# Kernel optimization log

Measured on AMD Instinct MI355X. Metric: run time of the kernel, lower is better.

The kernel has to match this reference:

```python
import jax, jax.numpy as jnp
import numpy as np

MAX_FREQ = 10
CORR_RADIUS = 2
PATCH = 9


def _gelu(x):
    return jax.nn.gelu(x, approximate=False)


def _project(coords, R, C0, f, pp):
    # coords [N,3] -> uv [ncams,N,2], cam-space z [ncams,N]
    d = coords[None, :, :] - C0[:, None, :]
    Xc = jnp.einsum('cij,cnj->cni', R, d)
    z = jnp.maximum(Xc[..., 2:3], 1e-6)
    uv = Xc[..., :2] / z * f[:, None, :] + pp[:, None, :]
    return uv, Xc[..., 2]


def _fourier(x, max_freq):
    freqs = (2.0 ** jnp.arange(max_freq, dtype=x.dtype)) * jnp.pi
    xf = x[..., None] * freqs
    enc = jnp.concatenate([jnp.sin(xf), jnp.cos(xf)], axis=-1)  # [...,D,2F]
    return enc.reshape(enc.shape[:-2] + (x.shape[-1] * 2 * max_freq,))


def _bilinear_time(img, t, gx, gy):
    # img [B,T,C,H,W]; t [B,K] int; gx,gy [B,K,P] normalized grid in [-1,1]
    # grid_sample(align_corners=False, padding_mode='zeros') via direct 4-tap gather
    B, T, C, H, W = img.shape
    x = (gx + 1.0) * 0.5 * W - 0.5
    y = (gy + 1.0) * 0.5 * H - 0.5
    x0 = jnp.floor(x)
    y0 = jnp.floor(y)
    wx = (x - x0)[..., None]
    wy = (y - y0)[..., None]
    x0 = x0.astype(jnp.int32)
    y0 = y0.astype(jnp.int32)
    b = jnp.arange(B)[:, None, None]
    tt = t[:, :, None]

    def tap(yy, xx):
        ok = ((xx >= 0) & (xx < W) & (yy >= 0) & (yy < H))[..., None]
        v = img[b, tt, :, jnp.clip(yy, 0, H - 1), jnp.clip(xx, 0, W - 1)]  # [B,K,P,C]
        return v * ok.astype(v.dtype)

    return (tap(y0, x0) * (1 - wx) * (1 - wy) + tap(y0, x0 + 1) * wx * (1 - wy)
            + tap(y0 + 1, x0) * (1 - wx) * wy + tap(y0 + 1, x0 + 1) * wx * wy)


def _conv2d(x, w, b):
    y = jax.lax.conv_general_dilated(x, w, (1, 1), 'SAME', dimension_numbers=('NCHW', 'OIHW', 'NCHW'))
    return y + b[None, :, None, None]


def _conv3d(x, w, b):
    y = jax.lax.conv_general_dilated(x, w, (1, 1, 1), 'SAME', dimension_numbers=('NCDHW', 'OIDHW', 'NCDHW'))
    return y + b[None, :, None, None, None]


def reference(views, cam_R, cam_center, cam_focal, cam_pp, query_coords, query_time, target_time, cube_scale, v2v_w, v2v_b, lin_vol_w, lin_vol_b, lin_pos_w, lin_pos_b, lin_depth_w, lin_depth_b, conv1_w, conv1_b, conv2_w, conv2_b, conv3_w, conv3_b, mlp1_w, mlp1_b, mlp2_w, mlp2_b, tq_emb, tt_emb, vis_emb_tab, depth_norm_scale, gate_w, gate_b, fus1_w, fus1_b, fus2_w, fus2_b):
    ncams, B, T, C, H, W = views.shape
    K = query_coords.shape[1]
    sizes = jnp.asarray([W, H], dtype=query_coords.dtype)

    # project query points to all cameras
    qflat = query_coords.reshape(-1, 3)
    p2d_flat, zc = _project(qflat, cam_R, cam_center, cam_focal, cam_pp)  # [ncams,BK,2]
    p2d_full = p2d_flat.reshape(ncams, B, K, 2)

    # fourier position embedding
    pp_n = jnp.transpose(p2d_full, (1, 2, 0, 3)) / sizes  # [B,K,ncams,2]
    embed_pos = _fourier(pp_n, MAX_FREQ) @ lin_pos_w.T + lin_pos_b

    # volume embedding: masked multi-camera cube sampling + 3D conv
    cs = 2 * CORR_RADIUS + 1
    P3 = cs ** 3
    row = (jnp.arange(cs, dtype=query_coords.dtype) - CORR_RADIUS) * (cube_scale * 2.0)
    gx3, gy3, gz3 = jnp.meshgrid(row, row, row, indexing='ij')
    xyz = jnp.stack([gx3, gy3, gz3], axis=-1).reshape(-1, 3)  # [P3,3], x outermost
    cube = (query_coords[:, :, None, :] + xyz).reshape(-1, 3)
    pc, _ = _project(cube, cam_R, cam_center, cam_focal, cam_pp)
    pc = pc.reshape(ncams, B, K, P3, 2)
    smps, msks = [], []
    for c in range(ncams):
        g = 2.0 * pc[c] / sizes - 1.0
        m = (g[..., 0] >= -1) & (g[..., 0] <= 1) & (g[..., 1] >= -1) & (g[..., 1] <= 1)
        s = _bilinear_time(views[c], query_time, g[..., 0], g[..., 1])  # [B,K,P3,C]
        smps.append(s)
        msks.append(m)
    vol = jnp.stack(smps)  # [ncams,B,K,P3,C]
    mf = jnp.stack(msks).astype(vol.dtype)[..., None]
    cnt = jnp.maximum(mf.sum(0), 1.0)
    mv = (vol * mf).sum(0) / cnt  # [B,K,P3,C]
    mv = mv.reshape(B, K, cs, cs, cs, C)  # (x,y,z,C)
    mv = jnp.transpose(mv, (0, 1, 5, 4, 3, 2)).reshape(B * K, C, cs, cs, cs)  # [(BK),C,z,y,x]
    mv = _gelu(_conv3d(mv, v2v_w, v2v_b))  # EmbedV2V: Conv3d(3,vdim,3) + GELU
    vd = mv.shape[1]
    mv = mv.reshape(B, K, vd, cs, cs, cs)
    mv = jnp.transpose(mv, (0, 1, 2, 5, 4, 3)).reshape(B, K, vd * P3)  # 'b t 1 (d total)'
    embed_volume = mv @ lin_vol_w.T + lin_vol_b
    embed_volume = jnp.broadcast_to(embed_volume[:, :, None, :], (B, K, ncams, embed_volume.shape[-1]))

    # patch embedding per camera
    lin = jnp.arange(PATCH, dtype=query_coords.dtype)
    gyy, gxx = jnp.meshgrid(lin, lin, indexing='ij')
    offs = jnp.stack([gxx - (PATCH - 1) / 2.0, gyy - (PATCH - 1) / 2.0], axis=-1)  # [P,P,2]
    pats = []
    for c in range(ncams):
        px = p2d_full[c][:, :, None, None, :] + offs  # [B,K,P,P,2]
        g = ((2.0 * px + 1.0) / sizes - 1.0).reshape(B, K, PATCH * PATCH, 2)
        s = _bilinear_time(views[c], query_time, g[..., 0], g[..., 1])  # [B,K,PP,C]
        pats.append(jnp.transpose(s.reshape(B, K, PATCH, PATCH, C), (0, 1, 4, 2, 3)))
    patches = jnp.stack(pats).reshape(ncams * B * K, C, PATCH, PATCH)
    x = _gelu(_conv2d(patches, conv1_w, conv1_b))
    x = _gelu(_conv2d(x, conv2_w, conv2_b))
    x = _gelu(_conv2d(x, conv3_w, conv3_b))
    x = x.reshape(x.shape[0], -1)  # 'b c p q -> b (c p q)'
    x = _gelu(x @ mlp1_w.T + mlp1_b)  # dropout is eval-mode identity
    emb_p = x @ mlp2_w.T + mlp2_b
    embed_patch = jnp.transpose(emb_p.reshape(ncams, B, K, -1), (1, 2, 0, 3))

    E = tq_emb.shape[1]
    embed_qt = jnp.broadcast_to(tq_emb[query_time][:, :, None, :], (B, K, ncams, E))
    embed_tt = jnp.broadcast_to(tt_emb[target_time][:, :, None, :], (B, K, ncams, E))

    # visibility (pinhole in-bounds check with margin=2)
    u = p2d_flat[..., 0]
    v = p2d_flat[..., 1]
    margin = 2.0
    vis = (zc > 0) & (u >= margin) & (u <= W - margin) & (v >= margin) & (v <= H - margin)
    vis = jnp.transpose(vis.reshape(ncams, B, K), (1, 2, 0))  # [B,K,ncams]
    embed_vis = vis_emb_tab[vis.astype(jnp.int32)]

    depths = jnp.linalg.norm(query_coords[:, :, None, :] - cam_center, axis=-1) / (cube_scale * depth_norm_scale[0])
    embed_depth = _fourier(depths[..., None], MAX_FREQ) @ lin_depth_w.T + lin_depth_b

    # gated fusion of 7 terms + fusion MLP
    terms = [embed_pos, embed_volume, embed_patch, embed_qt, embed_tt, embed_vis, embed_depth]
    gates = jax.nn.sigmoid(jnp.concatenate(terms, axis=-1) @ gate_w.T + gate_b)  # [B,K,ncams,7]
    fused = sum(gates[..., i:i + 1] * terms[i] for i in range(len(terms)))
    h = _gelu(fused @ fus1_w.T + fus1_b)
    embed_total = h @ fus2_w.T + fus2_b  # [B,K,ncams,decoder_dim]
    return embed_total, vis


def setup_inputs():
    ks = jax.random.split(jax.random.key(0), 24)
    ncams, B, T, C, H, W = 4, 2, 16, 3, 256, 256
    K, E, MF, cs, P, vdim = 256, 256, 10, 5, 9, 8
    views = jax.random.normal(ks[0], (ncams, B, T, C, H, W), jnp.float32)
    cam_R = jnp.tile(jnp.eye(3, dtype=jnp.float32)[None], (ncams, 1, 1))
    cam_center = jnp.stack([jnp.linspace(-0.5, 0.5, ncams), jnp.linspace(0.5, -0.5, ncams), jnp.full((ncams,), -5.0)], axis=-1).astype(jnp.float32)
    cam_focal = jnp.full((ncams, 2), 200.0, jnp.float32)
    cam_pp = jnp.full((ncams, 2), 128.0, jnp.float32)
    query_coords = jax.random.uniform(ks[1], (B, K, 3), jnp.float32, -1.0, 1.0)
    query_time = jax.random.randint(ks[2], (B, K), 0, T).astype(jnp.int32)
    target_time = jax.random.randint(ks[3], (B, K), 0, T).astype(jnp.int32)
    cube_scale = jnp.float32(0.02)

    def w(k, shape, s=0.02):
        return jax.random.normal(k, shape, jnp.float32) * s

    z = lambda n: jnp.zeros((n,), jnp.float32)
    return dict(
        views=views, cam_R=cam_R, cam_center=cam_center, cam_focal=cam_focal, cam_pp=cam_pp,
        query_coords=query_coords, query_time=query_time, target_time=target_time, cube_scale=cube_scale,
        v2v_w=w(ks[4], (vdim, C, 3, 3, 3)), v2v_b=z(vdim),
        lin_vol_w=w(ks[5], (E, cs ** 3 * vdim)), lin_vol_b=z(E),
        lin_pos_w=w(ks[6], (E, 4 * MF)), lin_pos_b=z(E),
        lin_depth_w=w(ks[7], (E, 2 * MF)), lin_depth_b=z(E),
        conv1_w=w(ks[8], (32, 3, 3, 3)), conv1_b=z(32),
        conv2_w=w(ks[9], (64, 32, 3, 3)), conv2_b=z(64),
        conv3_w=w(ks[10], (128, 64, 3, 3)), conv3_b=z(128),
        mlp1_w=w(ks[11], (2 * E, 128 * P * P)), mlp1_b=z(2 * E),
        mlp2_w=w(ks[12], (E, 2 * E)), mlp2_b=z(E),
        tq_emb=w(ks[13], (T, E), 1.0), tt_emb=w(ks[14], (T, E), 1.0),
        vis_emb_tab=w(ks[15], (2, E), 1.0),
        depth_norm_scale=jnp.array([500.0], jnp.float32),
        gate_w=w(ks[16], (7, 7 * E), 0.01), gate_b=z(7),
        fus1_w=w(ks[17], (4 * E, E)), fus1_b=z(4 * E),
        fus2_w=w(ks[18], (E, 4 * E)), fus2_b=z(E),
    )
```

## Files before the change

### kernel.cpp

```cpp
#include <hip/hip_runtime.h>
#include <hip/hip_bf16.h>

typedef __hip_bfloat16 bf16;
typedef __attribute__((ext_vector_type(8))) short short8;
typedef __attribute__((ext_vector_type(4))) float floatx4;

#define NC 4
#define BB 2
#define TS 16
#define CHN 3
#define HH 256
#define WW 256
#define KQ 256
#define EE 256
#define BKT 512
#define HW 65536
#define NSEG 25
#define CH1 32
#define CH1P 40
#define CH2 64
#define CH2P 72
#define PW 11

#define PB_WCL   32
#define PB_W23   160
#define PB_AUXW  416
#define PB_PROJ  424
#define PB_CUBE  936
#define PB_END   1960

__device__ __forceinline__ float tof(bf16 x){ return __bfloat162float(x); }
__device__ __forceinline__ bf16 tobf(float x){ return __float2bfloat16(x); }
__device__ __forceinline__ float gelu_f(float x){ return 0.5f*x*(1.f+erff(x*0.70710678118654752f)); }
__device__ __forceinline__ float ldx(const void* p, size_t i, int bf){
    return bf ? tof(((const bf16*)p)[i]) : ((const float*)p)[i];
}
__device__ __forceinline__ void gload_lds16(const void* g, void* l){
    __builtin_amdgcn_global_load_lds((const __attribute__((address_space(1))) void*)g,
                                     (__attribute__((address_space(3))) void*)l, 16, 0, 0);
}

struct CvtArgs { const void* src[NSEG]; int dstoff[NSEG]; int cnt[NSEG]; };

struct PrepArgs {
    const void *camF, *camR, *camC, *camP, *qc, *csc;
    const void *c2w, *c3w, *linv, *f1w, *f2w, *m2w, *m1w, *views;
    const void *v2vw, *v2vb;
    const int* qtime;
    bf16 *w2cl, *w3cl, *linv_bf, *f1w_bf, *f2w_bf, *m2w_bf, *m1w_bf;
    float *p2d, *visf;
    bf16* volf;
    void* dout;
    int* flagp;
};

__global__ __launch_bounds__(256) void prep_kernel(CvtArgs ca, float* __restrict__ pool, PrepArgs a)
{
    int bid = blockIdx.x, tid = threadIdx.x;
    int bf = (((const unsigned short*)a.camF)[0] != 0) ? 1 : 0;
    __shared__ float s_vol[3][7][7][7];
    __shared__ float s_ws[648];
    __shared__ float s_bs[8];

    if (bid < PB_WCL){
        for (int s=0; s<NSEG; ++s){
            const void* src = ca.src[s];
            float* d = pool + ca.dstoff[s];
            int n = ca.cnt[s];
            for (int i = bid*256 + tid; i < n; i += PB_WCL*256) d[i] = ldx(src, i, bf);
        }
    } else if (bid < PB_W23){
        int i0 = (bid-PB_WCL)*256 + tid;
        const int stride = (PB_W23-PB_WCL)*256;
        for (int i=i0; i<64*32*9; i+=stride){
            int oc=i/(32*9), r=i%(32*9), ic=r/9, tap=r%9;
            a.w2cl[tap*(64*CH1) + oc*CH1 + ic] = tobf(ldx(a.c2w, i, bf));
        }
        for (int i=i0; i<128*64*9; i+=stride){
            int oc=i/(64*9), r=i%(64*9), ic=r/9, tap=r%9;
            a.w3cl[tap*(128*CH2) + oc*CH2 + ic] = tobf(ldx(a.c3w, i, bf));
        }
    } else if (bid < PB_AUXW){
        int sub = (bid-PB_W23)>>6;
        int i0 = ((bid-PB_W23)&63)*256 + tid;
        const int stride = 64*256;
// ... 16 lines not shown
            int c = idx / BKT, bk = idx % BKT;
            float dx = ldx(a.qc,bk*3+0,bf) - ldx(a.camC,c*3+0,bf);
            float dy = ldx(a.qc,bk*3+1,bf) - ldx(a.camC,c*3+1,bf);
            float dz = ldx(a.qc,bk*3+2,bf) - ldx(a.camC,c*3+2,bf);
            float X0 = ldx(a.camR,c*9+0,bf)*dx + ldx(a.camR,c*9+1,bf)*dy + ldx(a.camR,c*9+2,bf)*dz;
            float X1 = ldx(a.camR,c*9+3,bf)*dx + ldx(a.camR,c*9+4,bf)*dy + ldx(a.camR,c*9+5,bf)*dz;
            float X2 = ldx(a.camR,c*9+6,bf)*dx + ldx(a.camR,c*9+7,bf)*dy + ldx(a.camR,c*9+8,bf)*dz;
            float z = fmaxf(X2, 1e-6f);
            float u = X0/z*ldx(a.camF,c*2+0,bf) + ldx(a.camP,c*2+0,bf);
            float v = X1/z*ldx(a.camF,c*2+1,bf) + ldx(a.camP,c*2+1,bf);
            a.p2d[idx*2+0] = u; a.p2d[idx*2+1] = v;
            bool vis = (X2 > 0.f) && (u >= 2.f) && (u <= (float)WW-2.f) && (v >= 2.f) && (v <= (float)HH-2.f);
            a.visf[idx] = vis ? 1.f : 0.f;
            float vv = vis ? 1.f : 0.f;
            size_t vidx = (size_t)BB*KQ*NC*EE + (size_t)bk*NC + c;
            if (bf) ((bf16*)a.dout)[vidx] = tobf(vv);
            else    ((float*)a.dout)[vidx] = vv;
        }
    } else if (bid < PB_CUBE){
        int bk = bid - PB_PROJ;
        int c = tid & 3;
        int pg = tid >> 2;
        int b = bk >> 8;
        for (int i=tid; i<3*343; i+=256) ((float*)s_vol)[i]=0.f;
        for (int i=tid; i<648; i+=256) s_ws[i]=ldx(a.v2vw,i,bf);
        if (tid<8) s_bs[tid]=ldx(a.v2vb,tid,bf);
        __syncthreads();
        float cs2 = ldx(a.csc,0,bf) * 2.f;
        int t = a.qtime[bk];
        float qx0 = ldx(a.qc,bk*3+0,bf);
        float qy0 = ldx(a.qc,bk*3+1,bf);
        float qz0 = ldx(a.qc,bk*3+2,bf);
        float R0=ldx(a.camR,c*9+0,bf), R1=ldx(a.camR,c*9+1,bf), R2=ldx(a.camR,c*9+2,bf);
        float R3=ldx(a.camR,c*9+3,bf), R4=ldx(a.camR,c*9+4,bf), R5=ldx(a.camR,c*9+5,bf);
        float R6=ldx(a.camR,c*9+6,bf), R7=ldx(a.camR,c*9+7,bf), R8=ldx(a.camR,c*9+8,bf);
        float Cx=ldx(a.camC,c*3+0,bf), Cy=ldx(a.camC,c*3+1,bf), Cz=ldx(a.camC,c*3+2,bf);
        float Fx=ldx(a.camF,c*2+0,bf), Fy=ldx(a.camF,c*2+1,bf);
        float Px=ldx(a.camP,c*2+0,bf), Py=ldx(a.camP,c*2+1,bf);
        #pragma unroll
        for (int pass=0; pass<2; ++pass){
            int p = (pass<<6) + pg;
            bool act = p < 125;
            int i=p/25, j=(p/5)%5, kz=p%5;
            float a0=0.f,a1=0.f,a2=0.f,ms=0.f;
            if (act){
                float qx = qx0 + (float)(i-2)*cs2;
                float qy = qy0 + (float)(j-2)*cs2;
                float qz = qz0 + (float)(kz-2)*cs2;
                float dx=qx-Cx, dy=qy-Cy, dz=qz-Cz;
// ... 11 lines not shown
                    size_t basev = (size_t)((c*BB+b)*TS + t)*CHN*HW;
                    float wxs[2]={1.f-wx,wx}, wys[2]={1.f-wy,wy};
                    #pragma unroll
                    for (int ty=0;ty<2;++ty){
                        int yy=iy+ty; if (yy<0||yy>=HH) continue;
                        #pragma unroll
                        for (int tx=0;tx<2;++tx){
                            int xx=ix+tx; if (xx<0||xx>=WW) continue;
                            float wt=wys[ty]*wxs[tx];
                            size_t o = basev + (size_t)yy*WW+xx;
                            a0 += wt*ldx(a.views,o,bf);
                            a1 += wt*ldx(a.views,o+HW,bf);
                            a2 += wt*ldx(a.views,o+2*HW,bf);
                        }
                    }
                }
            }
            a0 += __shfl_xor(a0,1); a0 += __shfl_xor(a0,2);
            a1 += __shfl_xor(a1,1); a1 += __shfl_xor(a1,2);
            a2 += __shfl_xor(a2,1); a2 += __shfl_xor(a2,2);
            ms += __shfl_xor(ms,1); ms += __shfl_xor(ms,2);
            if (act && c==0){
                float cnt = fmaxf(ms,1.f);
                s_vol[0][kz+1][j+1][i+1]=a0/cnt;
                s_vol[1][kz+1][j+1][i+1]=a1/cnt;
                s_vol[2][kz+1][j+1][i+1]=a2/cnt;
            }
        }
        __syncthreads();
        if (tid >= 104 && tid < 128) a.volf[bk*1024 + 1000 + (tid-104)] = tobf(0.f);
        if (tid < 125){
            int w2=tid/25, h2=(tid/5)%5, d2=tid%5;
            for (int oc=0;oc<8;++oc){
                float acc = s_bs[oc];
                #pragma unroll
                for (int ic=0;ic<3;++ic)
                  #pragma unroll
                  for (int dz=0;dz<3;++dz)
                    #pragma unroll
                    for (int dy=0;dy<3;++dy)
                      #pragma unroll
                      for (int dxx=0;dxx<3;++dxx)
                        acc += s_vol[ic][d2+dz][h2+dy][w2+dxx] * s_ws[(((oc*3+ic)*3+dz)*3+dy)*3+dxx];
                a.volf[bk*1024 + oc*125 + tid] = tobf(gelu_f(acc));
            }
        }
    } else {
        int i0 = (bid-PB_CUBE)*256 + tid;
        const int stride = (PB_END-PB_CUBE)*256;
        const int npair = (512*10368)/2;
        if (bf){
            const unsigned* s = (const unsigned*)a.m1w;
            unsigned* d = (unsigned*)a.m1w_bf;
            for (int i=i0; i<npair; i+=stride) d[i] = s[i];
        } else {
            const float2* s = (const float2*)a.m1w;
            unsigned* d = (unsigned*)a.m1w_bf;
            for (int i=i0; i<npair; i+=stride){
                float2 v = s[i];
                union { bf16 h[2]; unsigned u; } pk;
                pk.h[0]=tobf(v.x); pk.h[1]=tobf(v.y);
                d[i] = pk.u;
            }
        }
    }
}

__global__ __launch_bounds__(256) void patchconv_mfma_kernel(
    const void* __restrict__ views, const float* __restrict__ p2d,
    const int* __restrict__ qtime,
    const float* __restrict__ w1, const float* __restrict__ b1,
    const bf16* __restrict__ w2cl, const float* __restrict__ b2,
    const bf16* __restrict__ w3cl, const float* __restrict__ b3,
    bf16* __restrict__ act_out, int img0, const int* __restrict__ flagp)
{
    int img = img0 + blockIdx.x;
    int c = img>>9, b = (img>>8)&1, k = img&255;
    int bk = b*KQ + k;
    int tid = threadIdx.x;
    int wave = tid>>6, lane = tid&63;

    __shared__ __align__(16) bf16 a2cl[11*PW*CH2P];
    __shared__ __align__(16) bf16 a1cl[11*PW*CH1P];
    __shared__ float w1s[864];
    __shared__ float patch[3][11][11];

    for (int i=tid;i<3*11*11;i+=256) ((float*)patch)[i]=0.f;
    for (int i=tid;i<864;i+=256) w1s[i]=w1[i];
    {
        unsigned int* z1=(unsigned int*)a1cl; int n1 = 11*PW*CH1P/2;
        for (int i=tid;i<n1;i+=256) z1[i]=0u;
        unsigned int* z2=(unsigned int*)a2cl; int n2 = 11*PW*CH2P/2;
        for (int i=tid;i<n2;i+=256) z2[i]=0u;
    }
    __syncthreads();
    if (tid<243){
        int bf = *flagp;
        int ch = tid/81;
        int pp = tid - ch*81;
        float u=p2d[(c*BKT+bk)*2+0], v=p2d[(c*BKT+bk)*2+1];
        int t=qtime[bk];
        int r=pp/9,q=pp%9;
        float x=u+(float)(q-4), y=v+(float)(r-4);
        float xf=floorf(x), yf=floorf(y);
        int ix=(int)xf, iy=(int)yf;
        float wx=x-xf, wy=y-yf;
        size_t base = (size_t)((c*BB+b)*TS+t)*CHN*HW + (size_t)ch*HW;
        float acc=0.f;
        float wxs[2]={1.f-wx,wx}, wys[2]={1.f-wy,wy};
        #pragma unroll
        for (int ty=0;ty<2;++ty){
            int yy=iy+ty; if (yy<0||yy>=HH) continue;
            #pragma unroll
            for (int tx=0;tx<2;++tx){
                int xx=ix+tx; if (xx<0||xx>=WW) continue;
                acc += wys[ty]*wxs[tx]*ldx(views, base + (size_t)yy*WW+xx, bf);
            }
        }
        patch[ch][r+1][q+1]=acc;
    }
    __syncthreads();
    for (int o=tid;o<81*32;o+=256){
        int oc=o&31, pp=o>>5;
        int r=pp/9, q=pp-9*r;
        float acc=b1[oc];
        #pragma unroll
        for (int ic=0;ic<3;++ic)
          #pragma unroll
          for (int dy2=0;dy2<3;++dy2)
            #pragma unroll
            for (int dx2=0;dx2<3;++dx2)
              acc += patch[ic][r+dy2][q+dx2]*w1s[((oc*3+ic)*3+dy2)*3+dx2];
        a1cl[((r+1)*PW+(q+1))*CH1P + oc] = tobf(gelu_f(acc));
    }
    __syncthreads();
    int mrow = lane&15;
    int kgrp = lane>>4;
    int koff = kgrp<<3;
    {
        int baseoff[6];
        #pragma unroll
        for (int m=0;m<6;++m){
            int pos = m*16 + mrow; if (pos>80) pos=80;
            int r=pos/9, q=pos-9*r;
            baseoff[m] = (r*PW+q)*CH1P + koff;
        }
        floatx4 acc2[6];
        #pragma unroll
        for (int m=0;m<6;++m) acc2[m]=(floatx4){0.f,0.f,0.f,0.f};
        int n0 = wave<<4;
        #pragma unroll
        for (int tap=0; tap<9; ++tap){
            int dy=tap/3, dx=tap-3*dy;
            short8 bfrag = *(const short8*)(w2cl + ((size_t)tap*64 + n0 + mrow)*CH1 + koff);
            int toff = (dy*PW+dx)*CH1P;
            #pragma unroll
            for (int m=0;m<6;++m){
                short8 afrag = *(const short8*)&a1cl[baseoff[m]+toff];
                acc2[m] = __builtin_amdgcn_mfma_f32_16x16x32_bf16(afrag, bfrag, acc2[m], 0,0,0);
            }
        }
        int oc = n0 + mrow;
        float bb = b2[oc];
        #pragma unroll
        for (int m=0;m<6;++m){
            #pragma unroll
            for (int rg=0;rg<4;++rg){
                int pos = m*16 + (kgrp<<2)+rg;
                if (pos<=80){
                    int r=pos/9,q=pos-9*r;
                    a2cl[((r+1)*PW+(q+1))*CH2P + oc] = tobf(gelu_f(acc2[m][rg]+bb));
                }
            }
        }
    }
    __syncthreads();
    {
        int baseoff[6];
        #pragma unroll
        for (int m=0;m<6;++m){
            int pos = m*16 + mrow; if (pos>80) pos=80;
            int r=pos/9, q=pos-9*r;
            baseoff[m] = (r*PW+q)*CH2P;
        }
        floatx4 acc3[2][6];
        #pragma unroll
        for (int nt=0;nt<2;++nt)
          #pragma unroll
          for (int m=0;m<6;++m) acc3[nt][m]=(floatx4){0.f,0.f,0.f,0.f};
        int n0 = wave<<5;
        #pragma unroll
        for (int tap=0; tap<9; ++tap){
            int dy=tap/3, dx=tap-3*dy;
            int toff = (dy*PW+dx)*CH2P;
            #pragma unroll
            for (int ks=0;ks<2;++ks){
                int kof2 = (ks<<5) + koff;
                short8 b0 = *(const short8*)(w3cl + ((size_t)tap*128 + n0      + mrow)*CH2 + kof2);
                short8 b1f= *(const short8*)(w3cl + ((size_t)tap*128 + n0 + 16 + mrow)*CH2 + kof2);
                #pragma unroll
                for (int m=0;m<6;++m){
                    short8 af = *(const short8*)&a2cl[baseoff[m]+toff+kof2];
                    acc3[0][m] = __builtin_amdgcn_mfma_f32_16x16x32_bf16(af, b0,  acc3[0][m], 0,0,0);
                    acc3[1][m] = __builtin_amdgcn_mfma_f32_16x16x32_bf16(af, b1f, acc3[1][m], 0,0,0);
                }
            }
        }
        #pragma unroll
        for (int nt=0;nt<2;++nt){
            int oc = n0 + (nt<<4) + mrow;
            float bb = b3[oc];
            #pragma unroll
            for (int m=0;m<6;++m){
                #pragma unroll
                for (int rg=0;rg<4;++rg){
                    int pos = m*16 + (kgrp<<2)+rg;
                    if (pos<=80)
                        act_out[(size_t)blockIdx.x*10368 + oc*81 + pos] = tobf(gelu_f(acc3[nt][m][rg]+bb));
                }
            }
        }
    }
}

template<int OUT>
__global__ __launch_bounds__(256) void gemm_bf16_kernel(
    const bf16* __restrict__ A, const bf16* __restrict__ W, const float* __restrict__ bias,
    float* __restrict__ Cf, void* __restrict__ Cb, int M, int N, int K, int iters,
    int pstride, const int* __restrict__ flagp)
{
    __shared__ bf16 As[2][64][72];
    __shared__ bf16 Bs[2][64][72];
    int tid = threadIdx.x;
    int wave = tid>>6, lane = tid&63;
    int m0 = blockIdx.y<<6, n0 = blockIdx.x<<6;
    int kt0 = blockIdx.z*iters;
    int bfflag = (OUT==3) ? *flagp : 0;
    int lr = tid>>3;
    int lc = (tid&7)<<3;
    const bf16* Ap0 = A + (size_t)(m0+lr)*K    + (kt0<<6) + lc;
    const bf16* Ap1 = A + (size_t)(m0+lr+32)*K + (kt0<<6) + lc;
    const bf16* Wp0 = W + (size_t)(n0+lr)*K    + (kt0<<6) + lc;
    const bf16* Wp1 = W + (size_t)(n0+lr+32)*K + (kt0<<6) + lc;
    uint4 ra0 = *(const uint4*)Ap0;
    uint4 ra1 = *(const uint4*)Ap1;
    uint4 rb0 = *(const uint4*)Wp0;
    uint4 rb1 = *(const uint4*)Wp1;
    floatx4 acc[4];
    #pragma unroll
    for (int j=0;j<4;++j) acc[j] = (floatx4){0.f,0.f,0.f,0.f};
    int arow = (wave<<4) + (lane&15);
    int koff = (lane>>4)<<3;
    int nrow = lane&15;
    *(uint4*)&As[0][lr][lc]    = ra0;
    *(uint4*)&As[0][lr+32][lc] = ra1;
    *(uint4*)&Bs[0][lr][lc]    = rb0;
    *(uint4*)&Bs[0][lr+32][lc] = rb1;
    __syncthreads();
    for (int it=0; it<iters; ++it){
        int cur = it&1;
// ... 13 lines not shown
                acc[j] = __builtin_amdgcn_mfma_f32_16x16x32_bf16(af, bfr, acc[j], 0, 0, 0);
            }
        }
        if (it+1<iters){
            __syncthreads();
            int nxt = cur^1;
            *(uint4*)&As[nxt][lr][lc]    = ra0;
            *(uint4*)&As[nxt][lr+32][lc] = ra1;
            *(uint4*)&Bs[nxt][lr][lc]    = rb0;
            *(uint4*)&Bs[nxt][lr+32][lc] = rb1;
            __syncthreads();
        }
    }
    int crow = (wave<<4) + ((lane>>4)<<2);
    int ccol = lane&15;
    #pragma unroll
    for (int j=0;j<4;++j){
        int n = n0 + (j<<4) + ccol;
        if (OUT==1){
            float bb = bias[n];
            #pragma unroll
            for (int r=0;r<4;++r)
                ((bf16*)Cb)[(size_t)(m0+crow+r)*N + n] = tobf(gelu_f(acc[j][r] + bb));
        } else if (OUT==2){
            float* out = Cf + (size_t)blockIdx.z * pstride;
            #pragma unroll
            for (int r=0;r<4;++r)
                out[(size_t)(m0+crow+r)*N + n] = acc[j][r];
        } else {
            float bb = bias[n];
            #pragma unroll
            for (int r=0;r<4;++r){
                float v = acc[j][r] + bb;
                size_t ii = (size_t)(m0+crow+r)*N + n;
                if (bfflag) ((bf16*)Cb)[ii] = tobf(v);
                else        ((float*)Cb)[ii] = v;
            }
        }
    }
}

__global__ __launch_bounds__(256) void gemm128_kernel(
    const bf16* __restrict__ A, const bf16* __restrict__ W,
    float* __restrict__ Cf, int N, int K, int kiters_total, int zdiv, int pstride)
{
    __shared__ __align__(16) bf16 As[128][64];
    __shared__ __align__(16) bf16 Bs[128][64];
    int tid = threadIdx.x;
    int wave = tid>>6, lane = tid&63;
    int m0 = blockIdx.y<<7, n0 = blockIdx.x<<7;
    int it0 = (int)(((long)blockIdx.z     * kiters_total) / zdiv);
    int it1 = (int)(((long)(blockIdx.z+1) * kiters_total) / zdiv);
    float* out = Cf + (size_t)blockIdx.z * pstride;
    int srow = (wave<<5) + (lane>>3);
    int scol = (lane&7)<<3;
    const bf16* Ap = A + (size_t)(m0+srow)*K + ((size_t)it0<<6) + scol;
    const bf16* Bp = W + (size_t)(n0+srow)*K + ((size_t)it0<<6) + scol;
    bf16* AsW = &As[wave<<5][0];
    bf16* BsW = &Bs[wave<<5][0];
    floatx4 acc[4][4];
// ... 33 lines not shown
        int mrow = m0 + wm + (i<<4) + crow;
        #pragma unroll
        for (int j=0;j<4;++j){
            int n = n0 + wn + (j<<4) + ccol;
            #pragma unroll
            for (int r=0;r<4;++r)
                out[(size_t)(mrow+r)*N + n] = acc[i][j][r];
        }
    }
}

__global__ __launch_bounds__(256) void mlp1_fin_kernel(const float* __restrict__ P,
                                                       const float* __restrict__ bias,
                                                       bf16* __restrict__ Cb, int total, int Nmask,
                                                       int pstride){
    for (int i = blockIdx.x*256 + threadIdx.x; i < total; i += gridDim.x*256){
        float s = bias[i & Nmask];
        #pragma unroll
        for (int p=0;p<8;++p) s += P[(size_t)p*pstride + i];
        Cb[i] = tobf(gelu_f(s));
    }
}

__global__ __launch_bounds__(256) void terms_kernel(
    const float* __restrict__ p2d, const float* __restrict__ visf,
    const float* __restrict__ lvp, const float* __restrict__ linv_b,
    const float* __restrict__ embp, const float* __restrict__ m2_b,
    const float* __restrict__ lin_pos_w, const float* __restrict__ lin_pos_b,
    const float* __restrict__ lin_depth_w, const float* __restrict__ lin_depth_b,
    const float* __restrict__ tq_emb, const float* __restrict__ tt_emb,
    const float* __restrict__ vis_tab,
    const float* __restrict__ gate_w, const float* __restrict__ gate_b,
    const int* __restrict__ qtime, const int* __restrict__ ttime,
    const float* __restrict__ qc, const float* __restrict__ camC,
    const float* __restrict__ csc, const float* __restrict__ dns,
    bf16* __restrict__ fused)
{
    int row = blockIdx.x;
    int c = row & 3; int bk = row >> 2;
    int tid = threadIdx.x;
    __shared__ float feats[40];
    __shared__ float dfeat[20];
    __shared__ float terms[7][256];
    __shared__ float wred[4][7];
    __shared__ float gates_s[7];
    float u = p2d[(c*BKT+bk)*2+0], v = p2d[(c*BKT+bk)*2+1];
    if (tid < 40){
        int j = tid/20; int rem = tid%20;
        float xval = (j==0) ? u*(1.f/(float)WW) : v*(1.f/(float)HH);
        int fi = rem % 10; bool iscos = (rem >= 10);
        float arg = xval * (float)(1<<fi) * 3.14159265358979323846f;
        feats[tid] = iscos ? cosf(arg) : sinf(arg);
    } else if (tid < 60){
        int rem = tid-40;
        float dx = qc[bk*3+0]-camC[c*3+0];
        float dy = qc[bk*3+1]-camC[c*3+1];
        float dz = qc[bk*3+2]-camC[c*3+2];
        float dep = sqrtf(dx*dx+dy*dy+dz*dz) / (csc[0] * dns[0]);
        int fi = rem % 10; bool iscos = (rem >= 10);
        float arg = dep * (float)(1<<fi) * 3.14159265358979323846f;
        dfeat[rem] = iscos ? cosf(arg) : sinf(arg);
    }
    __syncthreads();
    int e = tid;
    float pos = lin_pos_b[e];
    for (int j2=0;j2<40;++j2) pos += feats[j2]*lin_pos_w[e*40+j2];
    float dep = lin_depth_b[e];
    for (int j2=0;j2<20;++j2) dep += dfeat[j2]*lin_depth_w[e*20+j2];
    float vol = linv_b[e];
    #pragma unroll
    for (int p=0;p<8;++p) vol += lvp[(size_t)p*(512*256) + bk*256+e];
    int img = (c*BB + (bk>>8))*KQ + (bk&255);
    float pat = embp[(size_t)img*256+e] + m2_b[e];
    int tq = qtime[bk], tt2 = ttime[bk];
    float qtv = tq_emb[tq*256+e];
    float ttv = tt_emb[tt2*256+e];
    int vb = (visf[c*BKT+bk] > 0.5f) ? 1 : 0;
    float viv = vis_tab[vb*256+e];
    terms[0][e]=pos; terms[1][e]=vol; terms[2][e]=pat; terms[3][e]=qtv;
    terms[4][e]=ttv; terms[5][e]=viv; terms[6][e]=dep;
    __syncthreads();
    float pg[7];
    #pragma unroll
    for (int g=0;g<7;++g) pg[g]=0.f;
    for (int j2=tid; j2<1792; j2+=256){
        float cv = ((const float*)terms)[j2];
        #pragma unroll
        for (int g=0;g<7;++g) pg[g] += cv * gate_w[g*1792 + j2];
    }
    #pragma unroll
    for (int g=0;g<7;++g){
        #pragma unroll
        for (int off=32; off>0; off>>=1) pg[g] += __shfl_down(pg[g], off, 64);
    }
    int wave = tid >> 6, lane = tid & 63;
    if (lane==0){
// ... 45 lines not shown
    float* P_c2b  = add(d_in[20],64);
    float* P_c3b  = add(d_in[22],128);
    float* P_m1b  = add(d_in[24],512);
    float* P_m2b  = add(d_in[26],256);
    float* P_tq   = add(d_in[27],4096);
    float* P_tt   = add(d_in[28],4096);
    float* P_vtab = add(d_in[29],512);
    float* P_gw   = add(d_in[31],12544);
    float* P_gb   = add(d_in[32],7);
    float* P_f1b  = add(d_in[34],1024);
    float* P_f2b  = add(d_in[36],256);

    bf16* m1w_bf = (bf16*)(base + 4185600);
    bf16* w2cl   = (bf16*)(base + 14802432);
    bf16* w3cl   = (bf16*)(base + 14839296);
    bf16* linv_bf= (bf16*)(base + 14986752);
    bf16* f1w_bf = (bf16*)(base + 15511040);
    bf16* f2w_bf = (bf16*)(base + 16035328);
    bf16* m2w_bf = (bf16*)(base + 16559616);
    float* p2d   = (float*)(base + 16821760);
    float* visf  = (float*)(base + 16838144);
    bf16*  volf_bf = (bf16*)(base + 16846336);
    float* lvparts = (float*)(base + 17894912);
    float* embp  = (float*)(base + 22089216);
    bf16*  mlp1o_bf = (bf16*)(base + 24186368);
    bf16*  fusedb_bf= (bf16*)(base + 26283520);
    int NCH = (ws_size >= 103353856ull) ? 1 : 2;
    int MCH = 2048 / NCH;
    bf16*  c3act   = (bf16*)(base + 27332096);
    bf16*  hbuf_bf = (bf16*)(base + 27332096);
    float* parts   = (float*)(base + 27332096 + (size_t)MCH*10368*2);

    PrepArgs pa;
    pa.camF=d_in[3]; pa.camR=d_in[1]; pa.camC=d_in[2]; pa.camP=d_in[4];
    pa.qc=d_in[5]; pa.csc=d_in[8];
    pa.c2w=d_in[19]; pa.c3w=d_in[21];
    pa.linv=d_in[11]; pa.f1w=d_in[33]; pa.f2w=d_in[35]; pa.m2w=d_in[25];
    pa.m1w=d_in[23]; pa.views=views;
    pa.v2vw=d_in[9]; pa.v2vb=d_in[10];
    pa.qtime=qtime;
    pa.w2cl=w2cl; pa.w3cl=w3cl; pa.linv_bf=linv_bf; pa.f1w_bf=f1w_bf;
    pa.f2w_bf=f2w_bf; pa.m2w_bf=m2w_bf; pa.m1w_bf=m1w_bf;
    pa.p2d=p2d; pa.visf=visf; pa.volf=volf_bf;
    pa.dout=d_out; pa.flagp=flag;

    prep_kernel<<<PB_END, 256, 0, stream>>>(ca, pool, pa);

    gemm_bf16_kernel<2><<<dim3(4,8,8), 256, 0, stream>>>(volf_bf, linv_bf, nullptr, lvparts, nullptr,
                                                         512, 256, 1024, 2, 512*256, nullptr);
    for (int ch=0; ch<NCH; ++ch){
        int img0 = ch*MCH;
        patchconv_mfma_kernel<<<MCH, 256, 0, stream>>>(views, p2d, qtime, P_c1w, P_c1b,
                                                       w2cl, P_c2b, w3cl, P_c3b, c3act, img0, flag);
        gemm128_kernel<<<dim3(4, MCH/128, 8), 256, 0, stream>>>(c3act, m1w_bf, parts,
                                                                512, 10368, 162, 8, MCH*512);
        mlp1_fin_kernel<<<512, 256, 0, stream>>>(parts, P_m1b, mlp1o_bf + (size_t)img0*512,
                                                 MCH*512, 511, MCH*512);
    }
    gemm_bf16_kernel<2><<<dim3(4,32,1), 256, 0, stream>>>(mlp1o_bf, m2w_bf, nullptr, embp, nullptr,
                                                          2048, 256, 512, 8, 0, nullptr);
    terms_kernel<<<2048, 256, 0, stream>>>(p2d, visf, lvparts, P_linvb, embp, P_m2b,
                                           P_linpw, P_linpb, P_lindw, P_lindb,
                                           P_tq, P_tt, P_vtab, P_gw, P_gb,
                                           qtime, ttime, P_qc, P_camC, P_csc, P_dns, fusedb_bf);
    gemm_bf16_kernel<1><<<dim3(16,32,1), 256, 0, stream>>>(fusedb_bf, f1w_bf, P_f1b, nullptr, hbuf_bf,
                                                           2048, 1024, 256, 4, 0, nullptr);
    gemm_bf16_kernel<3><<<dim3(4,32,1), 256, 0, stream>>>(hbuf_bf, f2w_bf, P_f2b, nullptr, d_out,
                                                          2048, 256, 1024, 16, 0, flag);
    (void)in_sizes; (void)n_in; (void)out_size;
}
```

Baseline: 414.6 us.

## Transpose conv3 output layout, fuse lin-vol GEMM into patchconv, split-K tail GEMMs

The mlp1 weight is now permuted in prep, staged through LDS, so the conv3 activations can be written position-major with packed 8-byte stores. Conv2 is written the same way, with the MFMA operands swapped. The lin-vol GEMM is folded into the patchconv launch as extra blocks to remove a dependency and a launch. The mlp2 and fus2 GEMMs use split-K with a separate finalize kernel, raising the number of blocks in flight. The costs are an extra kernel, extra partial-sum traffic, and a heavier prep block for the weight permutation.

```diff
diff --git a/kernel.cpp b/kernel.cpp
--- a/kernel.cpp
+++ b/kernel.cpp
@@ -27,7 +27,7 @@
 #define PB_AUXW  416
 #define PB_PROJ  424
 #define PB_CUBE  936
-#define PB_END   1960
+#define PB_END   1448
 
 __device__ __forceinline__ float tof(bf16 x){ return __bfloat162float(x); }
 __device__ __forceinline__ bf16 tobf(float x){ return __float2bfloat16(x); }
@@ -38,6 +38,9 @@
 __device__ __forceinline__ void gload_lds16(const void* g, void* l){
     __builtin_amdgcn_global_load_lds((const __attribute__((address_space(1))) void*)g,
                                      (__attribute__((address_space(3))) void*)l, 16, 0, 0);
+}
+__device__ __forceinline__ unsigned pack2(float a, float b){
+    union{ bf16 h[2]; unsigned u; } pk; pk.h[0]=tobf(a); pk.h[1]=tobf(b); return pk.u;
 }
 
 struct CvtArgs { const void* src[NSEG]; int dstoff[NSEG]; int cnt[NSEG]; };
@@ -54,13 +57,16 @@
     int* flagp;
 };
 
+union PrepSm {
+    struct { float vol[3][7][7][7]; float ws[648]; float bs[8]; } cube;
+    bf16 lin[10368];
+};
+
 __global__ __launch_bounds__(256) void prep_kernel(CvtArgs ca, float* __restrict__ pool, PrepArgs a)
 {
     int bid = blockIdx.x, tid = threadIdx.x;
     int bf = (((const unsigned short*)a.camF)[0] != 0) ? 1 : 0;
-    __shared__ float s_vol[3][7][7][7];
-    __shared__ float s_ws[648];
-    __shared__ float s_bs[8];
+    __shared__ PrepSm sm;
 
     if (bid < PB_WCL){
         for (int s=0; s<NSEG; ++s){
@@ -123,9 +129,9 @@
         int c = tid & 3;
         int pg = tid >> 2;
         int b = bk >> 8;
-        for (int i=tid; i<3*343; i+=256) ((float*)s_vol)[i]=0.f;
-        for (int i=tid; i<648; i+=256) s_ws[i]=ldx(a.v2vw,i,bf);
-        if (tid<8) s_bs[tid]=ldx(a.v2vb,tid,bf);
+        for (int i=tid; i<3*343; i+=256) ((float*)sm.cube.vol)[i]=0.f;
+        for (int i=tid; i<648; i+=256) sm.cube.ws[i]=ldx(a.v2vw,i,bf);
+        if (tid<8) sm.cube.bs[tid]=ldx(a.v2vb,tid,bf);
         __syncthreads();
         float cs2 = ldx(a.csc,0,bf) * 2.f;
         int t = a.qtime[bk];
@@ -183,9 +189,9 @@
             ms += __shfl_xor(ms,1); ms += __shfl_xor(ms,2);
             if (act && c==0){
                 float cnt = fmaxf(ms,1.f);
-                s_vol[0][kz+1][j+1][i+1]=a0/cnt;
-                s_vol[1][kz+1][j+1][i+1]=a1/cnt;
-                s_vol[2][kz+1][j+1][i+1]=a2/cnt;
+                sm.cube.vol[0][kz+1][j+1][i+1]=a0/cnt;
+                sm.cube.vol[1][kz+1][j+1][i+1]=a1/cnt;
+                sm.cube.vol[2][kz+1][j+1][i+1]=a2/cnt;
             }
         }
         __syncthreads();
@@ -193,7 +199,7 @@
         if (tid < 125){
             int w2=tid/25, h2=(tid/5)%5, d2=tid%5;
             for (int oc=0;oc<8;++oc){
-                float acc = s_bs[oc];
+                float acc = sm.cube.bs[oc];
                 #pragma unroll
                 for (int ic=0;ic<3;++ic)
                   #pragma unroll
@@ -202,56 +208,62 @@
                     for (int dy=0;dy<3;++dy)
                       #pragma unroll
                       for (int dxx=0;dxx<3;++dxx)
-                        acc += s_vol[ic][d2+dz][h2+dy][w2+dxx] * s_ws[(((oc*3+ic)*3+dz)*3+dy)*3+dxx];
+                        acc += sm.cube.vol[ic][d2+dz][h2+dy][w2+dxx] * sm.cube.ws[(((oc*3+ic)*3+dz)*3+dy)*3+dxx];
                 a.volf[bk*1024 + oc*125 + tid] = tobf(gelu_f(acc));
             }
         }
     } else {
-        int i0 = (bid-PB_CUBE)*256 + tid;
-        const int stride = (PB_END-PB_CUBE)*256;
-        const int npair = (512*10368)/2;
+        int n = bid - PB_CUBE;
+        const size_t off = (size_t)n*10368;
         if (bf){
-            const unsigned* s = (const unsigned*)a.m1w;
-            unsigned* d = (unsigned*)a.m1w_bf;
-            for (int i=i0; i<npair; i+=stride) d[i] = s[i];
+            const bf16* s = (const bf16*)a.m1w + off;
+            for (int i=tid;i<10368;i+=256) sm.lin[i]=s[i];
         } else {
-            const float2* s = (const float2*)a.m1w;
-            unsigned* d = (unsigned*)a.m1w_bf;
-            for (int i=i0; i<npair; i+=stride){
-                float2 v = s[i];
-                union { bf16 h[2]; unsigned u; } pk;
-                pk.h[0]=tobf(v.x); pk.h[1]=tobf(v.y);
-                d[i] = pk.u;
-            }
-        }
-    }
-}
-
-__global__ __launch_bounds__(256) void patchconv_mfma_kernel(
+            const float* s = (const float*)a.m1w + off;
+            for (int i=tid;i<10368;i+=256) sm.lin[i]=tobf(s[i]);
+        }
+        __syncthreads();
+        unsigned* d = (unsigned*)(a.m1w_bf + off);
+        for (int j2=tid; j2<5184; j2+=256){
+            int j = j2*2;
+            int pos0=j>>7, oc0=j&127;
+            int pos1=(j+1)>>7, oc1=(j+1)&127;
+            d[j2] = pack2(tof(sm.lin[oc0*81+pos0]), tof(sm.lin[oc1*81+pos1]));
+        }
+    }
+}
+
+struct __align__(16) PCShared {
+    bf16 a2cl[11*PW*CH2P];
+    bf16 a1cl[11*PW*CH1P];
+    float w1s[864];
+    float patch[3][11][11];
+};
+struct __align__(16) LVShared {
+    bf16 As[64][72];
+    bf16 Bs[64][72];
+};
+
+__device__ __forceinline__ void patchconv_body(
+    PCShared& sm, int img,
     const void* __restrict__ views, const float* __restrict__ p2d,
     const int* __restrict__ qtime,
     const float* __restrict__ w1, const float* __restrict__ b1,
     const bf16* __restrict__ w2cl, const float* __restrict__ b2,
     const bf16* __restrict__ w3cl, const float* __restrict__ b3,
-    bf16* __restrict__ act_out, int img0, const int* __restrict__ flagp)
+    bf16* __restrict__ act_out, const int* __restrict__ flagp)
 {
-    int img = img0 + blockIdx.x;
     int c = img>>9, b = (img>>8)&1, k = img&255;
     int bk = b*KQ + k;
     int tid = threadIdx.x;
     int wave = tid>>6, lane = tid&63;
 
-    __shared__ __align__(16) bf16 a2cl[11*PW*CH2P];
-    __shared__ __align__(16) bf16 a1cl[11*PW*CH1P];
-    __shared__ float w1s[864];
-    __shared__ float patch[3][11][11];
-
-    for (int i=tid;i<3*11*11;i+=256) ((float*)patch)[i]=0.f;
-    for (int i=tid;i<864;i+=256) w1s[i]=w1[i];
+    for (int i=tid;i<3*11*11;i+=256) ((float*)sm.patch)[i]=0.f;
+    for (int i=tid;i<864;i+=256) sm.w1s[i]=w1[i];
     {
-        unsigned int* z1=(unsigned int*)a1cl; int n1 = 11*PW*CH1P/2;
+        unsigned int* z1=(unsigned int*)sm.a1cl; int n1 = 11*PW*CH1P/2;
         for (int i=tid;i<n1;i+=256) z1[i]=0u;
-        unsigned int* z2=(unsigned int*)a2cl; int n2 = 11*PW*CH2P/2;
+        unsigned int* z2=(unsigned int*)sm.a2cl; int n2 = 11*PW*CH2P/2;
         for (int i=tid;i<n2;i+=256) z2[i]=0u;
     }
     __syncthreads();
@@ -278,7 +290,7 @@
                 acc += wys[ty]*wxs[tx]*ldx(views, base + (size_t)yy*WW+xx, bf);
             }
         }
-        patch[ch][r+1][q+1]=acc;
+        sm.patch[ch][r+1][q+1]=acc;
     }
     __syncthreads();
     for (int o=tid;o<81*32;o+=256){
@@ -291,8 +303,8 @@
           for (int dy2=0;dy2<3;++dy2)
             #pragma unroll
             for (int dx2=0;dx2<3;++dx2)
-              acc += patch[ic][r+dy2][q+dx2]*w1s[((oc*3+ic)*3+dy2)*3+dx2];
-        a1cl[((r+1)*PW+(q+1))*CH1P + oc] = tobf(gelu_f(acc));
+              acc += sm.patch[ic][r+dy2][q+dx2]*sm.w1s[((oc*3+ic)*3+dy2)*3+dx2];
+        sm.a1cl[((r+1)*PW+(q+1))*CH1P + oc] = tobf(gelu_f(acc));
     }
     __syncthreads();
     int mrow = lane&15;
@@ -313,25 +325,25 @@
         #pragma unroll
         for (int tap=0; tap<9; ++tap){
             int dy=tap/3, dx=tap-3*dy;
-            short8 bfrag = *(const short8*)(w2cl + ((size_t)tap*64 + n0 + mrow)*CH1 + koff);
+            short8 wfrag = *(const short8*)(w2cl + ((size_t)tap*64 + n0 + mrow)*CH1 + koff);
             int toff = (dy*PW+dx)*CH1P;
             #pragma unroll
             for (int m=0;m<6;++m){
-                short8 afrag = *(const short8*)&a1cl[baseoff[m]+toff];
-                acc2[m] = __builtin_amdgcn_mfma_f32_16x16x32_bf16(afrag, bfrag, acc2[m], 0,0,0);
-            }
-        }
-        int oc = n0 + mrow;
-        float bb = b2[oc];
+                short8 afrag = *(const short8*)&sm.a1cl[baseoff[m]+toff];
+                acc2[m] = __builtin_amdgcn_mfma_f32_16x16x32_bf16(wfrag, afrag, acc2[m], 0,0,0);
+            }
+        }
+        int ocb = n0 + (kgrp<<2);
+        float bb0=b2[ocb], bb1=b2[ocb+1], bb2=b2[ocb+2], bb3=b2[ocb+3];
         #pragma unroll
         for (int m=0;m<6;++m){
-            #pragma unroll
-            for (int rg=0;rg<4;++rg){
-                int pos = m*16 + (kgrp<<2)+rg;
-                if (pos<=80){
-                    int r=pos/9,q=pos-9*r;
-                    a2cl[((r+1)*PW+(q+1))*CH2P + oc] = tobf(gelu_f(acc2[m][rg]+bb));
-                }
+            int pos = m*16 + mrow;
+            if (pos<=80){
+                int r=pos/9,q=pos-9*r;
+                uint2 pk;
+                pk.x = pack2(gelu_f(acc2[m][0]+bb0), gelu_f(acc2[m][1]+bb1));
+                pk.y = pack2(gelu_f(acc2[m][2]+bb2), gelu_f(acc2[m][3]+bb3));
+                *(uint2*)&sm.a2cl[((r+1)*PW+(q+1))*CH2P + ocb] = pk;
             }
         }
     }
@@ -357,38 +369,119 @@
             #pragma unroll
             for (int ks=0;ks<2;++ks){
                 int kof2 = (ks<<5) + koff;
-                short8 b0 = *(const short8*)(w3cl + ((size_t)tap*128 + n0      + mrow)*CH2 + kof2);
-                short8 b1f= *(const short8*)(w3cl + ((size_t)tap*128 + n0 + 16 + mrow)*CH2 + kof2);
+                short8 w0 = *(const short8*)(w3cl + ((size_t)tap*128 + n0      + mrow)*CH2 + kof2);
+                short8 w1f= *(const short8*)(w3cl + ((size_t)tap*128 + n0 + 16 + mrow)*CH2 + kof2);
                 #pragma unroll
                 for (int m=0;m<6;++m){
-                    short8 af = *(const short8*)&a2cl[baseoff[m]+toff+kof2];
-                    acc3[0][m] = __builtin_amdgcn_mfma_f32_16x16x32_bf16(af, b0,  acc3[0][m], 0,0,0);
-                    acc3[1][m] = __builtin_amdgcn_mfma_f32_16x16x32_bf16(af, b1f, acc3[1][m], 0,0,0);
+                    short8 af = *(const short8*)&sm.a2cl[baseoff[m]+toff+kof2];
+                    acc3[0][m] = __builtin_amdgcn_mfma_f32_16x16x32_bf16(w0,  af, acc3[0][m], 0,0,0);
+                    acc3[1][m] = __builtin_amdgcn_mfma_f32_16x16x32_bf16(w1f, af, acc3[1][m], 0,0,0);
                 }
             }
         }
+        bf16* outp = act_out + (size_t)img*10368;
         #pragma unroll
         for (int nt=0;nt<2;++nt){
-            int oc = n0 + (nt<<4) + mrow;
-            float bb = b3[oc];
+            int ocb = n0 + (nt<<4) + (kgrp<<2);
+            float bb0=b3[ocb], bb1=b3[ocb+1], bb2=b3[ocb+2], bb3=b3[ocb+3];
             #pragma unroll
             for (int m=0;m<6;++m){
-                #pragma unroll
-                for (int rg=0;rg<4;++rg){
-                    int pos = m*16 + (kgrp<<2)+rg;
-                    if (pos<=80)
-                        act_out[(size_t)blockIdx.x*10368 + oc*81 + pos] = tobf(gelu_f(acc3[nt][m][rg]+bb));
+                int pos = m*16 + mrow;
+                if (pos<=80){
+                    uint2 pk;
+                    pk.x = pack2(gelu_f(acc3[nt][m][0]+bb0), gelu_f(acc3[nt][m][1]+bb1));
+                    pk.y = pack2(gelu_f(acc3[nt][m][2]+bb2), gelu_f(acc3[nt][m][3]+bb3));
+                    *(uint2*)&outp[pos*128 + ocb] = pk;
                 }
             }
         }
     }
+}
+
+__device__ __forceinline__ void linvol_body(
+    LVShared& sm, int r, const bf16* __restrict__ A, const bf16* __restrict__ W,
+    float* __restrict__ lvparts)
+{
+    int tid = threadIdx.x;
+    int wave = tid>>6, lane = tid&63;
+    int z = r>>5, rem = r&31, by = rem>>2, bx = rem&3;
+    int m0 = by<<6, n0 = bx<<6;
+    int kt0 = z*2;
+    int lr = tid>>3, lc = (tid&7)<<3;
+    floatx4 acc[4];
+    #pragma unroll
+    for (int j=0;j<4;++j) acc[j]=(floatx4){0.f,0.f,0.f,0.f};
+    int arow = (wave<<4) + (lane&15);
+    int koff = (lane>>4)<<3;
+    int nrow = lane&15;
+    for (int it=0; it<2; ++it){
+        int ko = (kt0+it)<<6;
+        *(uint4*)&sm.As[lr][lc]    = *(const uint4*)(A + (size_t)(m0+lr)*1024    + ko + lc);
+        *(uint4*)&sm.As[lr+32][lc] = *(const uint4*)(A + (size_t)(m0+lr+32)*1024 + ko + lc);
+        *(uint4*)&sm.Bs[lr][lc]    = *(const uint4*)(W + (size_t)(n0+lr)*1024    + ko + lc);
+        *(uint4*)&sm.Bs[lr+32][lc] = *(const uint4*)(W + (size_t)(n0+lr+32)*1024 + ko + lc);
+        __syncthreads();
+        #pragma unroll
+        for (int kk=0; kk<64; kk+=32){
+            short8 af = *(const short8*)&sm.As[arow][kk+koff];
+            #pragma unroll
+            for (int j=0;j<4;++j){
+                short8 wf = *(const short8*)&sm.Bs[(j<<4)+nrow][kk+koff];
+                acc[j] = __builtin_amdgcn_mfma_f32_16x16x32_bf16(af, wf, acc[j], 0,0,0);
+            }
+        }
+        __syncthreads();
+    }
+    float* out = lvparts + (size_t)z * (512*256);
+    int crow = (wave<<4) + ((lane>>4)<<2);
+    int ccol = lane&15;
+    #pragma unroll
+    for (int j=0;j<4;++j){
+        int n = n0 + (j<<4) + ccol;
+        #pragma unroll
+        for (int rr=0;rr<4;++rr)
+            out[(size_t)(m0+crow+rr)*256 + n] = acc[j][rr];
+    }
+}
+
+__global__ __launch_bounds__(256) void patchlin_kernel(
+    const void* __restrict__ views, const float* __restrict__ p2d,
+    const int* __restrict__ qtime,
+    const float* __restrict__ w1, const float* __restrict__ b1,
+    const bf16* __restrict__ w2cl, const float* __restrict__ b2,
+    const bf16* __restrict__ w3cl, const float* __restrict__ b3,
+    bf16* __restrict__ act_out, int img0, int npc, const int* __restrict__ flagp,
+    const bf16* __restrict__ volf, const bf16* __restrict__ linvw,
+    float* __restrict__ lvparts)
+{
+    __shared__ union { PCShared pc; LVShared lv; } sm;
+    int bid = blockIdx.x;
+    if (bid < npc){
+        patchconv_body(sm.pc, img0+bid, views, p2d, qtime, w1, b1, w2cl, b2, w3cl, b3,
+                       act_out, flagp);
+    } else {
+        linvol_body(sm.lv, bid-npc, volf, linvw, lvparts);
+    }
+}
+
+__global__ __launch_bounds__(256) void patchconv_kernel(
+    const void* __restrict__ views, const float* __restrict__ p2d,
+    const int* __restrict__ qtime,
+    const float* __restrict__ w1, const float* __restrict__ b1,
+    const bf16* __restrict__ w2cl, const float* __restrict__ b2,
+    const bf16* __restrict__ w3cl, const float* __restrict__ b3,
+    bf16* __restrict__ act_out, int img0, const int* __restrict__ flagp)
+{
+    __shared__ PCShared sm;
+    patchconv_body(sm, img0+blockIdx.x, views, p2d, qtime, w1, b1, w2cl, b2, w3cl, b3,
+                   act_out, flagp);
 }
 
 template<int OUT>
 __global__ __launch_bounds__(256) void gemm_bf16_kernel(
     const bf16* __restrict__ A, const bf16* __restrict__ W, const float* __restrict__ bias,
     float* __restrict__ Cf, void* __restrict__ Cb, int M, int N, int K, int iters,
-    int pstride, const int* __restrict__ flagp)
+    int pstride)
 {
     __shared__ bf16 As[2][64][72];
     __shared__ bf16 Bs[2][64][72];
@@ -396,7 +489,6 @@
     int wave = tid>>6, lane = tid&63;
     int m0 = blockIdx.y<<6, n0 = blockIdx.x<<6;
     int kt0 = blockIdx.z*iters;
-    int bfflag = (OUT==3) ? *flagp : 0;
     int lr = tid>>3;
     int lc = (tid&7)<<3;
     const bf16* Ap0 = A + (size_t)(m0+lr)*K    + (kt0<<6) + lc;
@@ -456,20 +548,11 @@
             #pragma unroll
             for (int r=0;r<4;++r)
                 ((bf16*)Cb)[(size_t)(m0+crow+r)*N + n] = tobf(gelu_f(acc[j][r] + bb));
-        } else if (OUT==2){
+        } else {
             float* out = Cf + (size_t)blockIdx.z * pstride;
             #pragma unroll
             for (int r=0;r<4;++r)
                 out[(size_t)(m0+crow+r)*N + n] = acc[j][r];
-        } else {
-            float bb = bias[n];
-            #pragma unroll
-            for (int r=0;r<4;++r){
-                float v = acc[j][r] + bb;
-                size_t ii = (size_t)(m0+crow+r)*N + n;
-                if (bfflag) ((bf16*)Cb)[ii] = tobf(v);
-                else        ((float*)Cb)[ii] = v;
-            }
         }
     }
 }
@@ -549,10 +632,24 @@
     }
 }
 
+__global__ __launch_bounds__(256) void fin2_kernel(const float* __restrict__ P,
+                                                   const float* __restrict__ bias,
+                                                   void* __restrict__ out, const int* __restrict__ flagp,
+                                                   int total, int mask, int pstride){
+    int bf = *flagp;
+    for (int i = blockIdx.x*256 + threadIdx.x; i < total; i += gridDim.x*256){
+        float s = bias[i & mask];
+        #pragma unroll
+        for (int p=0;p<4;++p) s += P[(size_t)p*pstride + i];
+        if (bf) ((bf16*)out)[i] = tobf(s);
+        else    ((float*)out)[i] = s;
+    }
+}
+
 __global__ __launch_bounds__(256) void terms_kernel(
     const float* __restrict__ p2d, const float* __restrict__ visf,
     const float* __restrict__ lvp, const float* __restrict__ linv_b,
-    const float* __restrict__ embp, const float* __restrict__ m2_b,
+    const float* __restrict__ m2p, const float* __restrict__ m2_b,
     const float* __restrict__ lin_pos_w, const float* __restrict__ lin_pos_b,
     const float* __restrict__ lin_depth_w, const float* __restrict__ lin_depth_b,
     const float* __restrict__ tq_emb, const float* __restrict__ tt_emb,
@@ -598,7 +695,7 @@
     #pragma unroll
     for (int p=0;p<8;++p) vol += lvp[(size_t)p*(512*256) + bk*256+e];
     int img = (c*BB + (bk>>8))*KQ + (bk&255);
-    float pat = embp[(size_t)img*256+e] + m2_b[e];
+    float pat = m2_b[e] + m2p[(size_t)img*256+e] + m2p[(size_t)(2048*256) + (size_t)img*256+e];
     int tq = qtime[bk], tt2 = ttime[bk];
     float qtv = tq_emb[tq*256+e];
     float ttv = tt_emb[tt2*256+e];
@@ -690,14 +787,15 @@
     float* visf  = (float*)(base + 16838144);
     bf16*  volf_bf = (bf16*)(base + 16846336);
     float* lvparts = (float*)(base + 17894912);
-    float* embp  = (float*)(base + 22089216);
     bf16*  mlp1o_bf = (bf16*)(base + 24186368);
     bf16*  fusedb_bf= (bf16*)(base + 26283520);
     int NCH = (ws_size >= 103353856ull) ? 1 : 2;
     int MCH = 2048 / NCH;
-    bf16*  c3act   = (bf16*)(base + 27332096);
-    bf16*  hbuf_bf = (bf16*)(base + 27332096);
-    float* parts   = (float*)(base + 27332096 + (size_t)MCH*10368*2);
+    bf16*  c3act    = (bf16*)(base + 27332096);
+    bf16*  hbuf_bf  = (bf16*)(base + 27332096);
+    float* m2parts  = (float*)(base + 31526400);
+    float* f2parts  = (float*)(base + 35720704);
+    float* parts    = (float*)(base + 27332096 + (size_t)MCH*10368*2);
 
     PrepArgs pa;
     pa.camF=d_in[3]; pa.camR=d_in[1]; pa.camC=d_in[2]; pa.camP=d_in[4];
@@ -714,26 +812,36 @@
 
     prep_kernel<<<PB_END, 256, 0, stream>>>(ca, pool, pa);
 
-    gemm_bf16_kernel<2><<<dim3(4,8,8), 256, 0, stream>>>(volf_bf, linv_bf, nullptr, lvparts, nullptr,
-                                                         512, 256, 1024, 2, 512*256, nullptr);
-    for (int ch=0; ch<NCH; ++ch){
-        int img0 = ch*MCH;
-        patchconv_mfma_kernel<<<MCH, 256, 0, stream>>>(views, p2d, qtime, P_c1w, P_c1b,
-                                                       w2cl, P_c2b, w3cl, P_c3b, c3act, img0, flag);
-        gemm128_kernel<<<dim3(4, MCH/128, 8), 256, 0, stream>>>(c3act, m1w_bf, parts,
-                                                                512, 10368, 162, 8, MCH*512);
-        mlp1_fin_kernel<<<512, 256, 0, stream>>>(parts, P_m1b, mlp1o_bf + (size_t)img0*512,
-                                                 MCH*512, 511, MCH*512);
-    }
-    gemm_bf16_kernel<2><<<dim3(4,32,1), 256, 0, stream>>>(mlp1o_bf, m2w_bf, nullptr, embp, nullptr,
-                                                          2048, 256, 512, 8, 0, nullptr);
-    terms_kernel<<<2048, 256, 0, stream>>>(p2d, visf, lvparts, P_linvb, embp, P_m2b,
+    if (NCH == 1){
+        patchlin_kernel<<<2048+256, 256, 0, stream>>>(views, p2d, qtime, P_c1w, P_c1b,
+                                                      w2cl, P_c2b, w3cl, P_c3b, c3act, 0, 2048, flag,
+                                                      volf_bf, linv_bf, lvparts);
+        gemm128_kernel<<<dim3(4, 16, 8), 256, 0, stream>>>(c3act, m1w_bf, parts,
+                                                           512, 10368, 162, 8, 2048*512);
+        mlp1_fin_kernel<<<512, 256, 0, stream>>>(parts, P_m1b, mlp1o_bf, 2048*512, 511, 2048*512);
+    } else {
+        gemm_bf16_kernel<2><<<dim3(4,8,8), 256, 0, stream>>>(volf_bf, linv_bf, nullptr, lvparts, nullptr,
+                                                             512, 256, 1024, 2, 512*256);
+        for (int ch=0; ch<NCH; ++ch){
+            int img0 = ch*MCH;
+            patchconv_kernel<<<MCH, 256, 0, stream>>>(views, p2d, qtime, P_c1w, P_c1b,
+                                                      w2cl, P_c2b, w3cl, P_c3b, c3act, img0, flag);
+            gemm128_kernel<<<dim3(4, MCH/128, 8), 256, 0, stream>>>(c3act, m1w_bf, parts,
+                                                                    512, 10368, 162, 8, MCH*512);
+            mlp1_fin_kernel<<<512, 256, 0, stream>>>(parts, P_m1b, mlp1o_bf + (size_t)img0*512,
+                                                     MCH*512, 511, MCH*512);
+        }
+    }
+    gemm_bf16_kernel<2><<<dim3(4,32,2), 256, 0, stream>>>(mlp1o_bf, m2w_bf, nullptr, m2parts, nullptr,
+                                                          2048, 256, 512, 4, 2048*256);
+    terms_kernel<<<2048, 256, 0, stream>>>(p2d, visf, lvparts, P_linvb, m2parts, P_m2b,
                                            P_linpw, P_linpb, P_lindw, P_lindb,
                                            P_tq, P_tt, P_vtab, P_gw, P_gb,
                                            qtime, ttime, P_qc, P_camC, P_csc, P_dns, fusedb_bf);
     gemm_bf16_kernel<1><<<dim3(16,32,1), 256, 0, stream>>>(fusedb_bf, f1w_bf, P_f1b, nullptr, hbuf_bf,
-                                                           2048, 1024, 256, 4, 0, nullptr);
-    gemm_bf16_kernel<3><<<dim3(4,32,1), 256, 0, stream>>>(hbuf_bf, f2w_bf, P_f2b, nullptr, d_out,
-                                                          2048, 256, 1024, 16, 0, flag);
+                                                           2048, 1024, 256, 4, 0);
+    gemm_bf16_kernel<2><<<dim3(4,32,4), 256, 0, stream>>>(hbuf_bf, f2w_bf, nullptr, f2parts, nullptr,
+                                                          2048, 256, 1024, 4, 2048*256);
+    fin2_kernel<<<512, 256, 0, stream>>>(f2parts, P_f2b, d_out, flag, 2048*256, 255, 2048*256);
     (void)in_sizes; (void)n_in; (void)out_size;
 }
```

After: 398.5 us. 1.04x faster.
